# Kernel optimization log

Hardware: AMD Instinct MI355X
Metric: run time of the kernel (lower is better)

Reference implementation:

```python
import jax, jax.numpy as jnp
import numpy as np

B, C, H, W = 8, 128, 64, 64
D_STATE = 16
D_CONV = 4
EXPAND = 1.25
D_INNER = int(EXPAND * C)        # 160
DT_RANK = int(np.ceil(C / 16))   # 8


def setup_inputs() -> dict:
    key = jax.random.key(0)
    ks = jax.random.split(key, 10)
    f = lambda k, s, sc=0.02: jax.random.normal(k, s, dtype=jnp.float32) * sc
    return {
        "x": jax.random.normal(ks[0], (B, C, H, W), dtype=jnp.float32),
        "ln_g": jnp.ones((C,), jnp.float32),
        "ln_b": jnp.zeros((C,), jnp.float32),
        "in_proj_w": f(ks[1], (2 * D_INNER, C)),
        "conv_w": f(ks[2], (D_INNER, 1, D_CONV)),            # depthwise causal conv kernel
        "conv_b": jnp.zeros((D_INNER,), jnp.float32),
        "x_proj_w": f(ks[3], (DT_RANK + 2 * D_STATE, D_INNER)),
        "dt_proj_w": f(ks[4], (D_INNER, DT_RANK), 0.1),
        "dt_proj_b": f(ks[5], (D_INNER,), 0.1),
        # S4-style init: A_log = log(1..d_state) per inner channel (frozen in torch module)
        "A_log": jnp.log(jnp.tile(jnp.arange(1, D_STATE + 1, dtype=jnp.float32), (D_INNER, 1))),
        "D_param": jnp.ones((D_INNER,), jnp.float32),
        "out_proj_w": f(ks[6], (C, D_INNER)),
        "fuse_w": f(ks[7], (C, 2 * C)),                      # 1x1 conv == per-token matmul
        "scale": jnp.ones((1,), jnp.float32) * 0.1,
    }


def _layernorm(x, g, b, eps=1e-5):
    m = x.mean(-1, keepdims=True)
    v = x.var(-1, keepdims=True)
    return (x - m) * jax.lax.rsqrt(v + eps) * g + b


def _mamba(seq, in_proj_w, conv_w, conv_b, x_proj_w, dt_proj_w, dt_proj_b,
           A_log, D_param, out_proj_w):
    # seq: (B, L, C)
    Bsz, L, _ = seq.shape
    xz = jnp.einsum('blc,ec->ble', seq, in_proj_w)           # (B, L, 2*d_inner)
    xm, z = jnp.split(xz, 2, axis=-1)
    # depthwise causal conv over L, truncated to L (padding = d_conv-1 on the left)
    xc = jax.lax.conv_general_dilated(
        xm.transpose(0, 2, 1), conv_w, (1,), [(D_CONV - 1, 0)],
        feature_group_count=D_INNER, dimension_numbers=('NCH', 'OIH', 'NCH'))
    xm = jax.nn.silu((xc + conv_b[None, :, None]).transpose(0, 2, 1))  # (B, L, d_inner)
    x_dbl = jnp.einsum('bld,ed->ble', xm, x_proj_w)
    dt = x_dbl[..., :DT_RANK]
    Bm = x_dbl[..., DT_RANK:DT_RANK + D_STATE]               # (B, L, d_state)
    Cm = x_dbl[..., DT_RANK + D_STATE:]                      # (B, L, d_state)
    dt = jax.nn.softplus(jnp.einsum('blr,dr->bld', dt, dt_proj_w) + dt_proj_b)
    A = -jnp.exp(A_log)                                      # (d_inner, d_state)

    def step(h, inp):
        dt_t, B_t, C_t, x_t = inp                            # (B,d) (B,n) (B,n) (B,d)
        dA = jnp.exp(dt_t[:, :, None] * A)                   # (B, d_inner, d_state)
        h = dA * h + (dt_t * x_t)[:, :, None] * B_t[:, None, :]
        y = jnp.einsum('bdn,bn->bd', h, C_t)
        return h, y

    h0 = jnp.zeros((Bsz, D_INNER, D_STATE), dtype=seq.dtype)
    xs = (dt.transpose(1, 0, 2), Bm.transpose(1, 0, 2),
          Cm.transpose(1, 0, 2), xm.transpose(1, 0, 2))
    _, ys = jax.lax.scan(step, h0, xs)                       # ys: (L, B, d_inner)
    y = ys.transpose(1, 0, 2) + xm * D_param
    y = y * jax.nn.silu(z)
    return jnp.einsum('bld,cd->blc', y, out_proj_w)          # (B, L, C)


def reference(x, ln_g, ln_b, in_proj_w, conv_w, conv_b, x_proj_w, dt_proj_w,
              dt_proj_b, A_log, D_param, out_proj_w, fuse_w, scale):
    Bsz, Ch, Hh, Ww = x.shape
    seq = x.reshape(Bsz, Ch, Hh * Ww).transpose(0, 2, 1)     # (B, L, C) raster order
    seq_n = _layernorm(seq, ln_g, ln_b)                      # LN is per-token: commutes with flip
    args = (in_proj_w, conv_w, conv_b, x_proj_w, dt_proj_w, dt_proj_b,
            A_log, D_param, out_proj_w)
    y0 = _mamba(seq_n, *args)                                # forward raster scan
    y1 = _mamba(seq_n[:, ::-1, :], *args)[:, ::-1, :]        # reversed raster scan
    fused = jnp.einsum('blk,ck->blc', jnp.concatenate([y0, y1], axis=-1), fuse_w)
    out = seq + scale * fused                                # residual + learned scale
    return out.transpose(0, 2, 1).reshape(Bsz, Ch, Hh, Ww)
```

## Files before the change

kernel.cpp:

```cpp
#include <hip/hip_runtime.h>
#include <math.h>

#define LSEQ   4096
#define BATCH  8
#define CDIM   128
#define DIN    160
#define DSTATE 16
#define DTRANK 8
#define BLROWS (BATCH*LSEQ)
#define NCHUNK 128
#define TCH    32
#define SUBC   8
#define NSEG   16

typedef __attribute__((ext_vector_type(8))) short short8;
typedef __attribute__((ext_vector_type(8))) __bf16 bf16x8;
typedef __attribute__((ext_vector_type(4))) float float4v;

__device__ __forceinline__ float4v mfma_bf16(short8 a, short8 b, float4v c) {
  return __builtin_amdgcn_mfma_f32_16x16x32_bf16(
      __builtin_bit_cast(bf16x8, a), __builtin_bit_cast(bf16x8, b), c, 0, 0, 0);
}

__device__ __forceinline__ unsigned short f2bf(float f) {
  union { float f; unsigned u; } v; v.f = f;
  unsigned r = v.u + 0x7FFF + ((v.u >> 16) & 1);
  return (unsigned short)(r >> 16);
}
__device__ __forceinline__ float bf2f(unsigned short h) {
  union { unsigned u; float f; } v; v.u = ((unsigned)h) << 16;
  return v.f;
}

__global__ void prep_weights(const float* __restrict__ inpw, const float* __restrict__ xpw,
                             const float* __restrict__ fuse_w, const float* __restrict__ out_proj_w,
                             unsigned short* __restrict__ inpw_bf, unsigned short* __restrict__ xpw_bf,
                             unsigned short* __restrict__ W01) {
  int i = blockIdx.x * 256 + threadIdx.x;
  if (i < 320 * 128) inpw_bf[i] = f2bf(inpw[i]);
  if (i < 40 * 160)  xpw_bf[i]  = f2bf(xpw[i]);
  if (i < CDIM * DIN) {
    int d = i % DIN, c = i / DIN;
    float a0 = 0.f, a1 = 0.f;
    for (int k = 0; k < CDIM; ++k) {
      float o = out_proj_w[k * DIN + d];
      a0 += fuse_w[c * 256 + k] * o;
      a1 += fuse_w[c * 256 + 128 + k] * o;
    }
    W01[c * DIN + d] = f2bf(a0);
    W01[CDIM * DIN + c * DIN + d] = f2bf(a1);
  }
}

__global__ void ln_transpose_kernel(const float* __restrict__ x,
                                    const float* __restrict__ g,
                                    const float* __restrict__ bb,
                                    unsigned short* __restrict__ seqn) {
  __shared__ float sA[128 * 65];
  __shared__ float psum[2 * 256];
  __shared__ float mrs[2 * 64];
  int l0 = blockIdx.x * 64;
  int b  = blockIdx.y;
  int t  = threadIdx.x;
  int lsub = t & 63, crow = t >> 6;
  const float* xb = x + (size_t)b * CDIM * LSEQ;
  for (int it = 0; it < 32; ++it) {
    int c = crow + it * 4;
    sA[c * 65 + lsub] = xb[(size_t)c * LSEQ + l0 + lsub];
  }
  __syncthreads();
  float s = 0.f, ss = 0.f;
  for (int j = 0; j < 32; ++j) {
    int c = crow * 32 + j;
    float v = sA[c * 65 + lsub];
    s += v; ss += v * v;
  }
  psum[crow * 64 + lsub] = s;
  psum[256 + crow * 64 + lsub] = ss;
  __syncthreads();
  if (t < 64) {
    float su = 0.f, sq = 0.f;
    for (int p = 0; p < 4; ++p) { su += psum[p * 64 + t]; sq += psum[256 + p * 64 + t]; }
    float m = su * (1.f / 128.f);
    float var = sq * (1.f / 128.f) - m * m;
    mrs[t] = m;
    mrs[64 + t] = rsqrtf(var + 1e-5f);
  }
  __syncthreads();
  int c = t & 127, half = t >> 7;
  float gc = g[c], bc = bb[c];
  for (int it = 0; it < 32; ++it) {
    int l = it * 2 + half;
    float v = (sA[c * 65 + l] - mrs[l]) * mrs[64 + l] * gc + bc;
    seqn[((size_t)(b * LSEQ + l0 + l)) * CDIM + c] = f2bf(v);
  }
}

template<int K, bool MASKN, bool BF16OUT>
__global__ __launch_bounds__(256)
void gemm_mfma(const unsigned short* __restrict__ A0, const unsigned short* __restrict__ A1,
               const unsigned short* __restrict__ W,
               void* __restrict__ C0, void* __restrict__ C1, int N) {
  constexpr int LSTR = K + 8;
  __shared__ __align__(16) unsigned short As[64 * LSTR];
  __shared__ __align__(16) unsigned short Ws[64 * LSTR];
  const unsigned short* A = blockIdx.z ? A1 : A0;
  void* Cp = blockIdx.z ? C1 : C0;
  int m0 = blockIdx.x * 64;
  int n0 = blockIdx.y * 64;
  int t = threadIdx.x;
  constexpr int CH = 64 * K / 8;
  for (int c = t; c < CH; c += 256) {
    int row = c / (K / 8);
    int col = (c % (K / 8)) * 8;
    *(short8*)&As[row * LSTR + col] = *(const short8*)&A[(size_t)(m0 + row) * K + col];
    short8 wv = {};
    int nr = n0 + row;
    if (!MASKN || nr < N) wv = *(const short8*)&W[(size_t)nr * K + col];
    *(short8*)&Ws[row * LSTR + col] = wv;
  }
  __syncthreads();
  int lane = t & 63;
  int w = t >> 6;
  int l15 = lane & 15, quad = lane >> 4;
  float4v acc[4] = {};
#pragma unroll
  for (int kk = 0; kk < K; kk += 32) {
    short8 bfrag = *(const short8*)&Ws[(w * 16 + l15) * LSTR + kk + quad * 8];
#pragma unroll
    for (int i = 0; i < 4; ++i) {
      short8 afrag = *(const short8*)&As[(i * 16 + l15) * LSTR + kk + quad * 8];
      acc[i] = mfma_bf16(afrag, bfrag, acc[i]);
    }
  }
  int col = n0 + w * 16 + l15;
  if (MASKN && col >= N) return;
#pragma unroll
  for (int i = 0; i < 4; ++i)
#pragma unroll
    for (int r = 0; r < 4; ++r) {
      int row = m0 + i * 16 + quad * 4 + r;
      if (BF16OUT) ((unsigned short*)Cp)[(size_t)row * N + col] = f2bf(acc[i][r]);
      else         ((float*)Cp)[(size_t)row * N + col] = acc[i][r];
    }
}

__global__ void conv_silu_kernel(const unsigned short* __restrict__ xz,
                                 const float* __restrict__ cw,
                                 const float* __restrict__ cb,
                                 unsigned short* __restrict__ xm0,
                                 unsigned short* __restrict__ xm1,
                                 _Float16* __restrict__ szp) {
  int idx = blockIdx.x * 256 + threadIdx.x;
  int dir = blockIdx.y;
  if (idx >= BLROWS * 80) return;
  int dp = idx % 80;
  int bl = idx / 80;
  int l = bl % LSEQ, b = bl / LSEQ;
  int d = dp * 2;
  float w0[4], w1[4];
#pragma unroll
  for (int k = 0; k < 4; ++k) { w0[k] = cw[d * 4 + k]; w1[k] = cw[d * 4 + 4 + k]; }
  float a0 = cb[d], a1 = cb[d + 1];
  const unsigned short* base = xz + ((size_t)b * LSEQ) * 320 + d;
  if (dir == 0) {
#pragma unroll
    for (int k = 0; k < 4; ++k) {
      int lp = l - 3 + k;
      if (lp >= 0) {
        unsigned v = *(const unsigned*)&base[(size_t)lp * 320];
        a0 += w0[k] * bf2f((unsigned short)v);
        a1 += w1[k] * bf2f((unsigned short)(v >> 16));
      }
    }
  } else {
#pragma unroll
    for (int k = 0; k < 4; ++k) {
      int lp = l + 3 - k;
      if (lp < LSEQ) {
        unsigned v = *(const unsigned*)&base[(size_t)lp * 320];
        a0 += w0[k] * bf2f((unsigned short)v);
        a1 += w1[k] * bf2f((unsigned short)(v >> 16));
      }
    }
  }
  float s0 = a0 * __builtin_amdgcn_rcpf(1.f + __expf(-a0));
  float s1 = a1 * __builtin_amdgcn_rcpf(1.f + __expf(-a1));
  unsigned outv = (unsigned)f2bf(s0) | ((unsigned)f2bf(s1) << 16);
  unsigned short* xm = dir ? xm1 : xm0;
  *(unsigned*)&xm[(size_t)bl * DIN + d] = outv;
  if (dir == 0) {
    unsigned zv = *(const unsigned*)&xz[(size_t)bl * 320 + 160 + d];
    float z0 = bf2f((unsigned short)zv), z1 = bf2f((unsigned short)(zv >> 16));
    float g0 = z0 * __builtin_amdgcn_rcpf(1.f + __expf(-z0));
    float g1 = z1 * __builtin_amdgcn_rcpf(1.f + __expf(-z1));
    unsigned short h0 = __builtin_bit_cast(unsigned short, (_Float16)g0);
    unsigned short h1 = __builtin_bit_cast(unsigned short, (_Float16)g1);
    *(unsigned*)&szp[(size_t)bl * DIN + d] = (unsigned)h0 | ((unsigned)h1 << 16);
  }
}

__device__ __forceinline__ void decay_powers(float r1, float* dA) {
  float r2 = r1 * r1;
  float r4 = r2 * r2;
  float r8 = r4 * r4;
  dA[0] = r1;       dA[1] = r2;       dA[2] = r2 * r1;  dA[3] = r4;
  dA[4] = r4 * r1;  dA[5] = r4 * r2;  dA[6] = r4 * dA[2]; dA[7] = r8;
  dA[8] = r8 * r1;  dA[9] = r8 * r2;  dA[10] = r8 * dA[2]; dA[11] = r8 * r4;
  dA[12] = r8 * dA[4]; dA[13] = r8 * dA[5]; dA[14] = r8 * dA[6]; dA[15] = r8 * r8;
}

__device__ __forceinline__ const float* uniform_row(const float* base, int elem_off) {
  return base + __builtin_amdgcn_readfirstlane(elem_off);
}

__global__ void scan_passA(const float* __restrict__ xdbl0, const float* __restrict__ xdbl1,
                           const unsigned short* __restrict__ xm0v, const unsigned short* __restrict__ xm1v,
                           const float* __restrict__ dt_w, const float* __restrict__ dt_b,
                           const float* __restrict__ Dp,
                           float* __restrict__ Q, float* __restrict__ dtsum,
                           unsigned* __restrict__ yr0, unsigned* __restrict__ yr1) {
  int chunk = blockIdx.x, b = blockIdx.y, dir = blockIdx.z;
  int t = threadIdx.x;
  if (t >= DIN) return;
  const float* xdbl = dir ? xdbl1 : xdbl0;
  const unsigned short* xm = dir ? xm1v : xm0v;
  unsigned* yr = dir ? yr1 : yr0;
  int d = t;
  float dw[8];
#pragma unroll
  for (int r = 0; r < 8; ++r) dw[r] = dt_w[d * 8 + r];
  float db = dt_b[d];
  float Dd = Dp[d];
  float h[16];
#pragma unroll
  for (int n = 0; n < 16; ++n) h[n] = 0.f;
  float cum = 0.f;
  float rcum = 1.f;
  int l00 = dir ? (LSEQ - 1 - chunk * TCH) : (chunk * TCH);
  int step = dir ? -1 : 1;
  int rowbase = b * LSEQ + l00;
  unsigned* yrp = yr + (size_t)rowbase * DIN + d;
#pragma unroll 4
  for (int tt = 0; tt < TCH; ++tt) {
    int rowi = rowbase + step * tt;
    const float* xr = uniform_row(xdbl, rowi * 40);
    float xmv = bf2f(xm[(size_t)rowi * DIN + d]);
    float za = db, zb = 0.f;
#pragma unroll
    for (int r = 0; r < 8; r += 2) { za += xr[r] * dw[r]; zb += xr[r + 1] * dw[r + 1]; }
    float zz = za + zb;
    float e  = __expf(fminf(zz, 20.f));
    float dt = (zz > 20.f) ? zz : __logf(1.f + e);
    float r1 = __builtin_amdgcn_rcpf(1.f + e);
    cum += dt;
    rcum *= r1;
    float u = dt * xmv;
    float dA[16];
    decay_powers(r1, dA);
#pragma unroll
    for (int n = 0; n < 16; ++n) h[n] = dA[n] * h[n] + u * xr[8 + n];
    float y0 = xmv * Dd, y1 = 0.f, y2 = 0.f, y3 = 0.f;
#pragma unroll
    for (int n = 0; n < 4; ++n) {
      y0 += h[n]      * xr[24 + n];
      y1 += h[4 + n]  * xr[28 + n];
      y2 += h[8 + n]  * xr[32 + n];
      y3 += h[12 + n] * xr[36 + n];
    }
    float y = (y0 + y1) + (y2 + y3);
    unsigned short rch = __builtin_bit_cast(unsigned short, (_Float16)rcum);
    *yrp = (unsigned)f2bf(y) | ((unsigned)rch << 16);
    yrp += step * DIN;
  }
  size_t base = (size_t)((dir * BATCH + b) * NCHUNK + chunk);
  float4v* qp = (float4v*)&Q[base * (DIN * 16) + d * 16];
#pragma unroll
  for (int n = 0; n < 4; ++n) {
    float4v qv = { h[4 * n], h[4 * n + 1], h[4 * n + 2], h[4 * n + 3] };
    qp[n] = qv;
  }
  dtsum[base * DIN + d] = cum;
}

__global__ __launch_bounds__(256)
void scan_passB(const float* Q, const float* __restrict__ dtsum,
                float* Hinit) {
  __shared__ float sA[NSEG * 16], sQ[NSEG * 16];
  int blk = blockIdx.x;
  int d = blk % DIN;
  int rem = blk / DIN;
  int t = threadIdx.x;
  int n = t & 15, cs = t >> 4;
  float An = -(float)(n + 1);
  float a[SUBC], q[SUBC];
  float Aseg = 1.f, Qseg = 0.f;
#pragma unroll
  for (int j = 0; j < SUBC; ++j) {
    int ch = cs * SUBC + j;
    size_t base = (size_t)rem * NCHUNK + ch;
    float dsv = dtsum[base * DIN + d];
    float av = __expf(An * dsv);
    float qv = Q[base * (DIN * 16) + d * 16 + n];
    a[j] = av; q[j] = qv;
    Qseg = av * Qseg + qv;
    Aseg *= av;
  }
  sA[cs * 16 + n] = Aseg;
  sQ[cs * 16 + n] = Qseg;
  __syncthreads();
  if (t < 16) {
    float h = 0.f;
    for (int s = 0; s < NSEG; ++s) {
      float Av = sA[s * 16 + t], Qv = sQ[s * 16 + t];
      sA[s * 16 + t] = h;
      h = Av * h + Qv;
    }
  }
  __syncthreads();
  float h = sA[cs * 16 + n];
#pragma unroll
  for (int j = 0; j < SUBC; ++j) {
    int ch = cs * SUBC + j;
    size_t base = (size_t)rem * NCHUNK + ch;
    Hinit[base * (DIN * 16) + d * 16 + n] = h;
    h = a[j] * h + q[j];
  }
}

__global__ void scan_passC(const float* __restrict__ xdbl0, const float* __restrict__ xdbl1,
                           const _Float16* __restrict__ szp,
                           const float* __restrict__ Hinit,
                           const unsigned* __restrict__ yr0, const unsigned* __restrict__ yr1,
                           unsigned short* __restrict__ yg0, unsigned short* __restrict__ yg1) {
  int chunk = blockIdx.x, b = blockIdx.y, dir = blockIdx.z;
  int t = threadIdx.x;
  if (t >= DIN) return;
  const float* xdbl = dir ? xdbl1 : xdbl0;
  const unsigned* yrb = dir ? yr1 : yr0;
  unsigned short* yg = dir ? yg1 : yg0;
  int d = t;
  size_t base = (size_t)((dir * BATCH + b) * NCHUNK + chunk);
  float H0[16];
  const float4v* hp = (const float4v*)&Hinit[base * (DIN * 16) + d * 16];
#pragma unroll
  for (int n = 0; n < 4; ++n) {
    float4v hv = hp[n];
    H0[4 * n] = hv[0]; H0[4 * n + 1] = hv[1]; H0[4 * n + 2] = hv[2]; H0[4 * n + 3] = hv[3];
  }
  int l00 = dir ? (LSEQ - 1 - chunk * TCH) : (chunk * TCH);
  int step = dir ? -1 : 1;
  int rowbase = b * LSEQ + l00;
  unsigned short* ygp = yg + (size_t)rowbase * DIN + d;
#pragma unroll 2
  for (int tt = 0; tt < TCH; ++tt) {
    int rowi = rowbase + step * tt;
    const float* xr = uniform_row(xdbl, rowi * 40 + 24);
    size_t di = (size_t)rowi * DIN + d;
    unsigned v = yrb[di];
    float y = bf2f((unsigned short)v);
    float rcum = (float)__builtin_bit_cast(_Float16, (unsigned short)(v >> 16));
    float sz = (float)szp[di];
    float dA[16];
    decay_powers(rcum, dA);
    float c0 = 0.f, c1 = 0.f, c2 = 0.f, c3 = 0.f;
#pragma unroll
    for (int n = 0; n < 4; ++n) {
      c0 += xr[n]      * (dA[n]      * H0[n]);
      c1 += xr[4 + n]  * (dA[4 + n]  * H0[4 + n]);
      c2 += xr[8 + n]  * (dA[8 + n]  * H0[8 + n]);
      c3 += xr[12 + n] * (dA[12 + n] * H0[12 + n]);
    }
    float corr = (c0 + c1) + (c2 + c3);
    *ygp = f2bf((y + corr) * sz);
    ygp += step * DIN;
  }
}

__global__ __launch_bounds__(256)
void final_mfma(const unsigned short* __restrict__ yg0, const unsigned short* __restrict__ yg1,
                const unsigned short* __restrict__ W01, const float* __restrict__ x,
                const float* __restrict__ scale, float* __restrict__ out) {
  constexpr int K = DIN, LSTR = K + 8;
  __shared__ __align__(16) unsigned short As[64 * LSTR];
  __shared__ __align__(16) unsigned short Ws[64 * LSTR];
  float* sC = (float*)As;
  int m0 = blockIdx.x * 64;
  int c0 = blockIdx.y * 64;
  int b = m0 / LSEQ, l0 = m0 % LSEQ;
  int t = threadIdx.x;
  int lane = t & 63;
  int w = t >> 6;
  int l15 = lane & 15, quad = lane >> 4;
  float4v acc[4] = {};
  for (int pass = 0; pass < 2; ++pass) {
    const unsigned short* A = pass ? yg1 : yg0;
    const unsigned short* W = W01 + pass * (CDIM * K);
    if (pass) __syncthreads();
    constexpr int CH = 64 * K / 8;
    for (int c = t; c < CH; c += 256) {
      int row = c / (K / 8);
      int col = (c % (K / 8)) * 8;
      *(short8*)&As[row * LSTR + col] = *(const short8*)&A[(size_t)(m0 + row) * K + col];
      *(short8*)&Ws[row * LSTR + col] = *(const short8*)&W[(size_t)(c0 + row) * K + col];
    }
    __syncthreads();
#pragma unroll
    for (int kk = 0; kk < K; kk += 32) {
      short8 bfrag = *(const short8*)&Ws[(w * 16 + l15) * LSTR + kk + quad * 8];
#pragma unroll
      for (int i = 0; i < 4; ++i) {
        short8 afrag = *(const short8*)&As[(i * 16 + l15) * LSTR + kk + quad * 8];
        acc[i] = mfma_bf16(afrag, bfrag, acc[i]);
      }
    }
  }
  __syncthreads();
#pragma unroll
  for (int i = 0; i < 4; ++i)
#pragma unroll
    for (int r = 0; r < 4; ++r)
      sC[(i * 16 + quad * 4 + r) * 65 + w * 16 + l15] = acc[i][r];
  __syncthreads();
  float sc = scale[0];
  int ll = t & 63, cq = t >> 6;
#pragma unroll
  for (int j = 0; j < 16; ++j) {
    int cl = cq * 16 + j;
    float v = sC[ll * 65 + cl];
    size_t gi = ((size_t)(b * CDIM + c0 + cl)) * LSEQ + l0 + ll;
    out[gi] = x[gi] + sc * v;
  }
}

extern "C" void kernel_launch(void* const* d_in, const int* in_sizes, int n_in,
                              void* d_out, int out_size, void* d_ws, size_t ws_size,
                              hipStream_t stream) {
  const float* x        = (const float*)d_in[0];
  const float* ln_g     = (const float*)d_in[1];
  const float* ln_b     = (const float*)d_in[2];
  const float* in_projw = (const float*)d_in[3];
  const float* conv_w   = (const float*)d_in[4];
  const float* conv_b   = (const float*)d_in[5];
  const float* x_projw  = (const float*)d_in[6];
  const float* dt_projw = (const float*)d_in[7];
  const float* dt_projb = (const float*)d_in[8];
  const float* A_log    = (const float*)d_in[9];
  const float* D_param  = (const float*)d_in[10];
  const float* out_projw= (const float*)d_in[11];
  const float* fuse_w   = (const float*)d_in[12];
  const float* scale    = (const float*)d_in[13];
  float* out = (float*)d_out;
  (void)A_log;

  float* ws = (float*)d_ws;
  size_t off = 0;
  unsigned short* seqn_bf = (unsigned short*)(ws + off); off += (size_t)BLROWS * CDIM / 2;
  unsigned short* xz      = (unsigned short*)(ws + off); off += (size_t)BLROWS * 320 / 2;
  unsigned short* xm0 = (unsigned short*)(ws + off); off += (size_t)BLROWS * DIN / 2;
  unsigned short* xm1 = (unsigned short*)(ws + off); off += (size_t)BLROWS * DIN / 2;
  float* xdbl0 = ws + off; off += (size_t)BLROWS * 40;
  float* xdbl1 = ws + off; off += (size_t)BLROWS * 40;
  float* Q     = ws + off; off += (size_t)2 * BATCH * NCHUNK * DIN * 16;
  float* Hinit = Q;
  float* dtsum = ws + off; off += (size_t)2 * BATCH * NCHUNK * DIN;
  unsigned* yr0 = (unsigned*)(ws + off); off += (size_t)BLROWS * DIN;
  unsigned* yr1 = (unsigned*)(ws + off); off += (size_t)BLROWS * DIN;
  unsigned short* yg0 = (unsigned short*)(ws + off); off += (size_t)BLROWS * DIN / 2;
  unsigned short* yg1 = (unsigned short*)(ws + off); off += (size_t)BLROWS * DIN / 2;
  _Float16* szv = (_Float16*)(ws + off); off += (size_t)BLROWS * DIN / 2;
  unsigned short* W01bf = (unsigned short*)(ws + off); off += (size_t)2 * CDIM * DIN / 2;
  unsigned short* inpw_bf = (unsigned short*)(ws + off); off += (size_t)320 * 128 / 2;
  unsigned short* xpw_bf  = (unsigned short*)(ws + off); off += (size_t)40 * 160 / 2 + 8;

  prep_weights<<<(320 * 128 + 255) / 256, 256, 0, stream>>>(
      in_projw, x_projw, fuse_w, out_projw, inpw_bf, xpw_bf, W01bf);
  ln_transpose_kernel<<<dim3(LSEQ / 64, BATCH), 256, 0, stream>>>(x, ln_g, ln_b, seqn_bf);
  gemm_mfma<128, false, true><<<dim3(BLROWS / 64, 5, 1), 256, 0, stream>>>(
      seqn_bf, seqn_bf, inpw_bf, xz, xz, 320);
  conv_silu_kernel<<<dim3((BLROWS * 80 + 255) / 256, 2), 256, 0, stream>>>(
      xz, conv_w, conv_b, xm0, xm1, szv);
  gemm_mfma<160, true, false><<<dim3(BLROWS / 64, 1, 2), 256, 0, stream>>>(
      xm0, xm1, xpw_bf, xdbl0, xdbl1, 40);
  scan_passA<<<dim3(NCHUNK, BATCH, 2), 192, 0, stream>>>(xdbl0, xdbl1, xm0, xm1,
                                                         dt_projw, dt_projb, D_param,
                                                         Q, dtsum, yr0, yr1);
  scan_passB<<<2 * BATCH * DIN, 256, 0, stream>>>(Q, dtsum, Hinit);
  scan_passC<<<dim3(NCHUNK, BATCH, 2), 192, 0, stream>>>(xdbl0, xdbl1, szv, Hinit,
                                                         yr0, yr1, yg0, yg1);
  final_mfma<<<dim3(BLROWS / 64, CDIM / 64), 256, 0, stream>>>(yg0, yg1, W01bf, x, scale, out);
}
```

Measured before the change: 248.0 us.

## Fold dt_proj into x_proj GEMM and precompute softplus inputs for scan

Precomposes dt_proj with the dt rows of x_proj into a 192x160 weight, so the x-projection GEMM directly produces the dt pre-activation. Its epilogue applies softplus and the decay factor, then stores packed fp16 (u, r1) pairs along with separate B/C values. The scan passes stage B/C for the chunk in shared memory, prefetch per-step operands eight steps ahead, and replace the dtsum exp in pass B with powers of the cumulative decay. This removes the per-step dt projection and transcendentals from the serial scan, at the cost of a larger GEMM, extra fp16 traffic, reduced precision for u and r1, and reuse of the xz buffer for UR0.

```diff
diff --git a/kernel.cpp b/kernel.cpp
--- a/kernel.cpp
+++ b/kernel.cpp
@@ -31,14 +31,31 @@
   union { unsigned u; float f; } v; v.u = ((unsigned)h) << 16;
   return v.f;
 }
+__device__ __forceinline__ float f16tof(unsigned short h) {
+  return (float)__builtin_bit_cast(_Float16, h);
+}
+__device__ __forceinline__ unsigned short ftof16(float f) {
+  return __builtin_bit_cast(unsigned short, (_Float16)f);
+}
 
 __global__ void prep_weights(const float* __restrict__ inpw, const float* __restrict__ xpw,
+                             const float* __restrict__ dtw,
                              const float* __restrict__ fuse_w, const float* __restrict__ out_proj_w,
-                             unsigned short* __restrict__ inpw_bf, unsigned short* __restrict__ xpw_bf,
+                             unsigned short* __restrict__ inpw_bf, unsigned short* __restrict__ Wx,
                              unsigned short* __restrict__ W01) {
   int i = blockIdx.x * 256 + threadIdx.x;
   if (i < 320 * 128) inpw_bf[i] = f2bf(inpw[i]);
-  if (i < 40 * 160)  xpw_bf[i]  = f2bf(xpw[i]);
+  if (i < 192 * 160) {
+    int rw = i / 160, e = i - rw * 160;
+    float v;
+    if (rw < 160) {
+      v = 0.f;
+      for (int r = 0; r < 8; ++r) v += dtw[rw * 8 + r] * xpw[r * 160 + e];
+    } else {
+      v = xpw[(rw - 160 + 8) * 160 + e];
+    }
+    Wx[i] = f2bf(v);
+  }
   if (i < CDIM * DIN) {
     int d = i % DIN, c = i / DIN;
     float a0 = 0.f, a1 = 0.f;
@@ -145,6 +162,70 @@
     }
 }
 
+__global__ __launch_bounds__(256)
+void gemm_xproj(const unsigned short* __restrict__ A0, const unsigned short* __restrict__ A1,
+                const unsigned short* __restrict__ W, const float* __restrict__ dt_b,
+                unsigned* __restrict__ UR0, unsigned* __restrict__ UR1,
+                float* __restrict__ BCo0, float* __restrict__ BCo1) {
+  constexpr int K = DIN, LSTR = K + 8;
+  __shared__ __align__(16) unsigned short As[64 * LSTR];
+  __shared__ __align__(16) unsigned short Ws[64 * LSTR];
+  const unsigned short* A = blockIdx.z ? A1 : A0;
+  unsigned* UR = blockIdx.z ? UR1 : UR0;
+  float* BCo = blockIdx.z ? BCo1 : BCo0;
+  int m0 = blockIdx.x * 64;
+  int n0 = blockIdx.y * 64;
+  int t = threadIdx.x;
+  constexpr int CH = 64 * K / 8;
+  for (int c = t; c < CH; c += 256) {
+    int row = c / (K / 8);
+    int col = (c % (K / 8)) * 8;
+    *(short8*)&As[row * LSTR + col] = *(const short8*)&A[(size_t)(m0 + row) * K + col];
+    *(short8*)&Ws[row * LSTR + col] = *(const short8*)&W[(size_t)(n0 + row) * K + col];
+  }
+  __syncthreads();
+  int lane = t & 63;
+  int w = t >> 6;
+  int l15 = lane & 15, quad = lane >> 4;
+  float4v acc[4] = {};
+#pragma unroll
+  for (int kk = 0; kk < K; kk += 32) {
+    short8 bfrag = *(const short8*)&Ws[(w * 16 + l15) * LSTR + kk + quad * 8];
+#pragma unroll
+    for (int i = 0; i < 4; ++i) {
+      short8 afrag = *(const short8*)&As[(i * 16 + l15) * LSTR + kk + quad * 8];
+      acc[i] = mfma_bf16(afrag, bfrag, acc[i]);
+    }
+  }
+  int col = n0 + w * 16 + l15;
+  if (col < 160) {
+    float db = dt_b[col];
+#pragma unroll
+    for (int i = 0; i < 4; ++i)
+#pragma unroll
+      for (int r = 0; r < 4; ++r) {
+        int rl = i * 16 + quad * 4 + r;
+        int row = m0 + rl;
+        float zz = acc[i][r] + db;
+        float e  = __expf(fminf(zz, 20.f));
+        float dt = (zz > 20.f) ? zz : __logf(1.f + e);
+        float r1 = __builtin_amdgcn_rcpf(1.f + e);
+        float xmv = bf2f(As[rl * LSTR + col]);
+        float u = dt * xmv;
+        UR[(size_t)row * DIN + col] = (unsigned)ftof16(u) | ((unsigned)ftof16(r1) << 16);
+      }
+  } else {
+    int c2 = col - 160;
+#pragma unroll
+    for (int i = 0; i < 4; ++i)
+#pragma unroll
+      for (int r = 0; r < 4; ++r) {
+        int row = m0 + i * 16 + quad * 4 + r;
+        BCo[(size_t)row * 32 + c2] = acc[i][r];
+      }
+  }
+}
+
 __global__ void conv_silu_kernel(const unsigned short* __restrict__ xz,
                                  const float* __restrict__ cw,
                                  const float* __restrict__ cb,
@@ -194,9 +275,7 @@
     float z0 = bf2f((unsigned short)zv), z1 = bf2f((unsigned short)(zv >> 16));
     float g0 = z0 * __builtin_amdgcn_rcpf(1.f + __expf(-z0));
     float g1 = z1 * __builtin_amdgcn_rcpf(1.f + __expf(-z1));
-    unsigned short h0 = __builtin_bit_cast(unsigned short, (_Float16)g0);
-    unsigned short h1 = __builtin_bit_cast(unsigned short, (_Float16)g1);
-    *(unsigned*)&szp[(size_t)bl * DIN + d] = (unsigned)h0 | ((unsigned)h1 << 16);
+    *(unsigned*)&szp[(size_t)bl * DIN + d] = (unsigned)ftof16(g0) | ((unsigned)ftof16(g1) << 16);
   }
 }
 
@@ -210,68 +289,69 @@
   dA[12] = r8 * dA[4]; dA[13] = r8 * dA[5]; dA[14] = r8 * dA[6]; dA[15] = r8 * r8;
 }
 
-__device__ __forceinline__ const float* uniform_row(const float* base, int elem_off) {
-  return base + __builtin_amdgcn_readfirstlane(elem_off);
-}
-
-__global__ void scan_passA(const float* __restrict__ xdbl0, const float* __restrict__ xdbl1,
-                           const unsigned short* __restrict__ xm0v, const unsigned short* __restrict__ xm1v,
-                           const float* __restrict__ dt_w, const float* __restrict__ dt_b,
-                           const float* __restrict__ Dp,
-                           float* __restrict__ Q, float* __restrict__ dtsum,
-                           unsigned* __restrict__ yr0, unsigned* __restrict__ yr1) {
+__global__ __launch_bounds__(192)
+void scan_passA(const float* __restrict__ BC0, const float* __restrict__ BC1,
+                const unsigned* __restrict__ UR0, const unsigned* __restrict__ UR1,
+                const unsigned short* __restrict__ xm0v, const unsigned short* __restrict__ xm1v,
+                const float* __restrict__ Dp,
+                float* __restrict__ Q, float* __restrict__ rcf,
+                unsigned* __restrict__ yr0, unsigned* __restrict__ yr1) {
+  __shared__ __align__(16) float sBC[TCH * 32];
   int chunk = blockIdx.x, b = blockIdx.y, dir = blockIdx.z;
   int t = threadIdx.x;
-  if (t >= DIN) return;
-  const float* xdbl = dir ? xdbl1 : xdbl0;
+  const float* BC = dir ? BC1 : BC0;
+  const unsigned* UR = dir ? UR1 : UR0;
   const unsigned short* xm = dir ? xm1v : xm0v;
   unsigned* yr = dir ? yr1 : yr0;
-  int d = t;
-  float dw[8];
-#pragma unroll
-  for (int r = 0; r < 8; ++r) dw[r] = dt_w[d * 8 + r];
-  float db = dt_b[d];
-  float Dd = Dp[d];
-  float h[16];
-#pragma unroll
-  for (int n = 0; n < 16; ++n) h[n] = 0.f;
-  float cum = 0.f;
-  float rcum = 1.f;
   int l00 = dir ? (LSEQ - 1 - chunk * TCH) : (chunk * TCH);
   int step = dir ? -1 : 1;
   int rowbase = b * LSEQ + l00;
+  for (int i = t; i < TCH * 32; i += 192)
+    sBC[i] = BC[(size_t)(rowbase + step * (i >> 5)) * 32 + (i & 31)];
+  __syncthreads();
+  if (t >= DIN) return;
+  int d = t;
+  float Dd = Dp[d];
+  float h[16];
+#pragma unroll
+  for (int n = 0; n < 16; ++n) h[n] = 0.f;
+  float rcum = 1.f;
+  const unsigned* urp = UR + (size_t)rowbase * DIN + d;
+  const unsigned short* xmp = xm + (size_t)rowbase * DIN + d;
   unsigned* yrp = yr + (size_t)rowbase * DIN + d;
-#pragma unroll 4
-  for (int tt = 0; tt < TCH; ++tt) {
-    int rowi = rowbase + step * tt;
-    const float* xr = uniform_row(xdbl, rowi * 40);
-    float xmv = bf2f(xm[(size_t)rowi * DIN + d]);
-    float za = db, zb = 0.f;
-#pragma unroll
-    for (int r = 0; r < 8; r += 2) { za += xr[r] * dw[r]; zb += xr[r + 1] * dw[r + 1]; }
-    float zz = za + zb;
-    float e  = __expf(fminf(zz, 20.f));
-    float dt = (zz > 20.f) ? zz : __logf(1.f + e);
-    float r1 = __builtin_amdgcn_rcpf(1.f + e);
-    cum += dt;
-    rcum *= r1;
-    float u = dt * xmv;
-    float dA[16];
-    decay_powers(r1, dA);
-#pragma unroll
-    for (int n = 0; n < 16; ++n) h[n] = dA[n] * h[n] + u * xr[8 + n];
-    float y0 = xmv * Dd, y1 = 0.f, y2 = 0.f, y3 = 0.f;
-#pragma unroll
-    for (int n = 0; n < 4; ++n) {
-      y0 += h[n]      * xr[24 + n];
-      y1 += h[4 + n]  * xr[28 + n];
-      y2 += h[8 + n]  * xr[32 + n];
-      y3 += h[12 + n] * xr[36 + n];
-    }
-    float y = (y0 + y1) + (y2 + y3);
-    unsigned short rch = __builtin_bit_cast(unsigned short, (_Float16)rcum);
-    *yrp = (unsigned)f2bf(y) | ((unsigned)rch << 16);
-    yrp += step * DIN;
+  int sstep = step * DIN;
+  unsigned urb[8]; unsigned short xmb[8];
+#pragma unroll
+  for (int j = 0; j < 8; ++j) { urb[j] = urp[sstep * j]; xmb[j] = xmp[sstep * j]; }
+  for (int g = 0; g < TCH / 8; ++g) {
+#pragma unroll
+    for (int j = 0; j < 8; ++j) {
+      int tt = g * 8 + j;
+      unsigned urv = urb[j];
+      float xmv = bf2f(xmb[j]);
+      if (g < TCH / 8 - 1) {
+        urb[j] = urp[sstep * (tt + 8)];
+        xmb[j] = xmp[sstep * (tt + 8)];
+      }
+      float u  = f16tof((unsigned short)(urv & 0xFFFF));
+      float r1 = f16tof((unsigned short)(urv >> 16));
+      rcum *= r1;
+      float dA[16];
+      decay_powers(r1, dA);
+      const float* br = &sBC[tt * 32];
+#pragma unroll
+      for (int n = 0; n < 16; ++n) h[n] = dA[n] * h[n] + u * br[n];
+      float y0 = xmv * Dd, y1 = 0.f, y2 = 0.f, y3 = 0.f;
+#pragma unroll
+      for (int n = 0; n < 4; ++n) {
+        y0 += h[n]      * br[16 + n];
+        y1 += h[4 + n]  * br[20 + n];
+        y2 += h[8 + n]  * br[24 + n];
+        y3 += h[12 + n] * br[28 + n];
+      }
+      float y = (y0 + y1) + (y2 + y3);
+      yrp[sstep * tt] = (unsigned)f2bf(y) | ((unsigned)ftof16(rcum) << 16);
+    }
   }
   size_t base = (size_t)((dir * BATCH + b) * NCHUNK + chunk);
   float4v* qp = (float4v*)&Q[base * (DIN * 16) + d * 16];
@@ -280,11 +360,11 @@
     float4v qv = { h[4 * n], h[4 * n + 1], h[4 * n + 2], h[4 * n + 3] };
     qp[n] = qv;
   }
-  dtsum[base * DIN + d] = cum;
+  rcf[base * DIN + d] = rcum;
 }
 
 __global__ __launch_bounds__(256)
-void scan_passB(const float* Q, const float* __restrict__ dtsum,
+void scan_passB(const float* Q, const float* __restrict__ rcf,
                 float* Hinit) {
   __shared__ float sA[NSEG * 16], sQ[NSEG * 16];
   int blk = blockIdx.x;
@@ -292,15 +372,21 @@
   int rem = blk / DIN;
   int t = threadIdx.x;
   int n = t & 15, cs = t >> 4;
-  float An = -(float)(n + 1);
+  unsigned k = n + 1;
   float a[SUBC], q[SUBC];
   float Aseg = 1.f, Qseg = 0.f;
 #pragma unroll
   for (int j = 0; j < SUBC; ++j) {
     int ch = cs * SUBC + j;
     size_t base = (size_t)rem * NCHUNK + ch;
-    float dsv = dtsum[base * DIN + d];
-    float av = __expf(An * dsv);
+    float rf = rcf[base * DIN + d];
+    float r2 = rf * rf, r4 = r2 * r2, r8 = r4 * r4;
+    float av = 1.f;
+    if (k & 1) av *= rf;
+    if (k & 2) av *= r2;
+    if (k & 4) av *= r4;
+    if (k & 8) av *= r8;
+    if (k & 16) av = r8 * r8;
     float qv = Q[base * (DIN * 16) + d * 16 + n];
     a[j] = av; q[j] = qv;
     Qseg = av * Qseg + qv;
@@ -328,17 +414,25 @@
   }
 }
 
-__global__ void scan_passC(const float* __restrict__ xdbl0, const float* __restrict__ xdbl1,
-                           const _Float16* __restrict__ szp,
-                           const float* __restrict__ Hinit,
-                           const unsigned* __restrict__ yr0, const unsigned* __restrict__ yr1,
-                           unsigned short* __restrict__ yg0, unsigned short* __restrict__ yg1) {
+__global__ __launch_bounds__(192)
+void scan_passC(const float* __restrict__ BC0, const float* __restrict__ BC1,
+                const _Float16* __restrict__ szp,
+                const float* __restrict__ Hinit,
+                const unsigned* __restrict__ yr0, const unsigned* __restrict__ yr1,
+                unsigned short* __restrict__ yg0, unsigned short* __restrict__ yg1) {
+  __shared__ __align__(16) float sC[TCH * 16];
   int chunk = blockIdx.x, b = blockIdx.y, dir = blockIdx.z;
   int t = threadIdx.x;
+  const float* BC = dir ? BC1 : BC0;
+  const unsigned* yrb0 = dir ? yr1 : yr0;
+  unsigned short* yg = dir ? yg1 : yg0;
+  int l00 = dir ? (LSEQ - 1 - chunk * TCH) : (chunk * TCH);
+  int step = dir ? -1 : 1;
+  int rowbase = b * LSEQ + l00;
+  for (int i = t; i < TCH * 16; i += 192)
+    sC[i] = BC[(size_t)(rowbase + step * (i >> 4)) * 32 + 16 + (i & 15)];
+  __syncthreads();
   if (t >= DIN) return;
-  const float* xdbl = dir ? xdbl1 : xdbl0;
-  const unsigned* yrb = dir ? yr1 : yr0;
-  unsigned short* yg = dir ? yg1 : yg0;
   int d = t;
   size_t base = (size_t)((dir * BATCH + b) * NCHUNK + chunk);
   float H0[16];
@@ -348,32 +442,39 @@
     float4v hv = hp[n];
     H0[4 * n] = hv[0]; H0[4 * n + 1] = hv[1]; H0[4 * n + 2] = hv[2]; H0[4 * n + 3] = hv[3];
   }
-  int l00 = dir ? (LSEQ - 1 - chunk * TCH) : (chunk * TCH);
-  int step = dir ? -1 : 1;
-  int rowbase = b * LSEQ + l00;
+  const unsigned* yrp = yrb0 + (size_t)rowbase * DIN + d;
+  const unsigned short* szq = (const unsigned short*)szp + (size_t)rowbase * DIN + d;
   unsigned short* ygp = yg + (size_t)rowbase * DIN + d;
-#pragma unroll 2
-  for (int tt = 0; tt < TCH; ++tt) {
-    int rowi = rowbase + step * tt;
-    const float* xr = uniform_row(xdbl, rowi * 40 + 24);
-    size_t di = (size_t)rowi * DIN + d;
-    unsigned v = yrb[di];
-    float y = bf2f((unsigned short)v);
-    float rcum = (float)__builtin_bit_cast(_Float16, (unsigned short)(v >> 16));
-    float sz = (float)szp[di];
-    float dA[16];
-    decay_powers(rcum, dA);
-    float c0 = 0.f, c1 = 0.f, c2 = 0.f, c3 = 0.f;
-#pragma unroll
-    for (int n = 0; n < 4; ++n) {
-      c0 += xr[n]      * (dA[n]      * H0[n]);
-      c1 += xr[4 + n]  * (dA[4 + n]  * H0[4 + n]);
-      c2 += xr[8 + n]  * (dA[8 + n]  * H0[8 + n]);
-      c3 += xr[12 + n] * (dA[12 + n] * H0[12 + n]);
-    }
-    float corr = (c0 + c1) + (c2 + c3);
-    *ygp = f2bf((y + corr) * sz);
-    ygp += step * DIN;
+  int sstep = step * DIN;
+  unsigned yb[8]; unsigned short sb[8];
+#pragma unroll
+  for (int j = 0; j < 8; ++j) { yb[j] = yrp[sstep * j]; sb[j] = szq[sstep * j]; }
+  for (int g = 0; g < TCH / 8; ++g) {
+#pragma unroll
+    for (int j = 0; j < 8; ++j) {
+      int tt = g * 8 + j;
+      unsigned v = yb[j];
+      float sz = f16tof(sb[j]);
+      if (g < TCH / 8 - 1) {
+        yb[j] = yrp[sstep * (tt + 8)];
+        sb[j] = szq[sstep * (tt + 8)];
+      }
+      float y = bf2f((unsigned short)v);
+      float rcum = f16tof((unsigned short)(v >> 16));
+      const float* cr = &sC[tt * 16];
+      float dA[16];
+      decay_powers(rcum, dA);
+      float c0 = 0.f, c1 = 0.f, c2 = 0.f, c3 = 0.f;
+#pragma unroll
+      for (int n = 0; n < 4; ++n) {
+        c0 += cr[n]      * (dA[n]      * H0[n]);
+        c1 += cr[4 + n]  * (dA[4 + n]  * H0[4 + n]);
+        c2 += cr[8 + n]  * (dA[8 + n]  * H0[8 + n]);
+        c3 += cr[12 + n] * (dA[12 + n] * H0[12 + n]);
+      }
+      float corr = (c0 + c1) + (c2 + c3);
+      ygp[sstep * tt] = f2bf((y + corr) * sz);
+    }
   }
 }
 
@@ -457,36 +558,37 @@
   size_t off = 0;
   unsigned short* seqn_bf = (unsigned short*)(ws + off); off += (size_t)BLROWS * CDIM / 2;
   unsigned short* xz      = (unsigned short*)(ws + off); off += (size_t)BLROWS * 320 / 2;
+  unsigned* UR0 = (unsigned*)xz;
   unsigned short* xm0 = (unsigned short*)(ws + off); off += (size_t)BLROWS * DIN / 2;
   unsigned short* xm1 = (unsigned short*)(ws + off); off += (size_t)BLROWS * DIN / 2;
-  float* xdbl0 = ws + off; off += (size_t)BLROWS * 40;
-  float* xdbl1 = ws + off; off += (size_t)BLROWS * 40;
+  float* BC0 = ws + off; off += (size_t)BLROWS * 32;
+  float* BC1 = ws + off; off += (size_t)BLROWS * 32;
   float* Q     = ws + off; off += (size_t)2 * BATCH * NCHUNK * DIN * 16;
   float* Hinit = Q;
-  float* dtsum = ws + off; off += (size_t)2 * BATCH * NCHUNK * DIN;
+  float* rcf   = ws + off; off += (size_t)2 * BATCH * NCHUNK * DIN;
   unsigned* yr0 = (unsigned*)(ws + off); off += (size_t)BLROWS * DIN;
   unsigned* yr1 = (unsigned*)(ws + off); off += (size_t)BLROWS * DIN;
   unsigned short* yg0 = (unsigned short*)(ws + off); off += (size_t)BLROWS * DIN / 2;
   unsigned short* yg1 = (unsigned short*)(ws + off); off += (size_t)BLROWS * DIN / 2;
   _Float16* szv = (_Float16*)(ws + off); off += (size_t)BLROWS * DIN / 2;
+  unsigned* UR1 = (unsigned*)(ws + off); off += (size_t)BLROWS * DIN;
   unsigned short* W01bf = (unsigned short*)(ws + off); off += (size_t)2 * CDIM * DIN / 2;
   unsigned short* inpw_bf = (unsigned short*)(ws + off); off += (size_t)320 * 128 / 2;
-  unsigned short* xpw_bf  = (unsigned short*)(ws + off); off += (size_t)40 * 160 / 2 + 8;
+  unsigned short* Wx_bf   = (unsigned short*)(ws + off); off += (size_t)192 * 160 / 2 + 8;
 
   prep_weights<<<(320 * 128 + 255) / 256, 256, 0, stream>>>(
-      in_projw, x_projw, fuse_w, out_projw, inpw_bf, xpw_bf, W01bf);
+      in_projw, x_projw, dt_projw, fuse_w, out_projw, inpw_bf, Wx_bf, W01bf);
   ln_transpose_kernel<<<dim3(LSEQ / 64, BATCH), 256, 0, stream>>>(x, ln_g, ln_b, seqn_bf);
   gemm_mfma<128, false, true><<<dim3(BLROWS / 64, 5, 1), 256, 0, stream>>>(
       seqn_bf, seqn_bf, inpw_bf, xz, xz, 320);
   conv_silu_kernel<<<dim3((BLROWS * 80 + 255) / 256, 2), 256, 0, stream>>>(
       xz, conv_w, conv_b, xm0, xm1, szv);
-  gemm_mfma<160, true, false><<<dim3(BLROWS / 64, 1, 2), 256, 0, stream>>>(
-      xm0, xm1, xpw_bf, xdbl0, xdbl1, 40);
-  scan_passA<<<dim3(NCHUNK, BATCH, 2), 192, 0, stream>>>(xdbl0, xdbl1, xm0, xm1,
-                                                         dt_projw, dt_projb, D_param,
-                                                         Q, dtsum, yr0, yr1);
-  scan_passB<<<2 * BATCH * DIN, 256, 0, stream>>>(Q, dtsum, Hinit);
-  scan_passC<<<dim3(NCHUNK, BATCH, 2), 192, 0, stream>>>(xdbl0, xdbl1, szv, Hinit,
+  gemm_xproj<<<dim3(BLROWS / 64, 3, 2), 256, 0, stream>>>(
+      xm0, xm1, Wx_bf, dt_projb, UR0, UR1, BC0, BC1);
+  scan_passA<<<dim3(NCHUNK, BATCH, 2), 192, 0, stream>>>(BC0, BC1, UR0, UR1, xm0, xm1,
+                                                         D_param, Q, rcf, yr0, yr1);
+  scan_passB<<<2 * BATCH * DIN, 256, 0, stream>>>(Q, rcf, Hinit);
+  scan_passC<<<dim3(NCHUNK, BATCH, 2), 192, 0, stream>>>(BC0, BC1, szv, Hinit,
                                                          yr0, yr1, yg0, yg1);
   final_mfma<<<dim3(BLROWS / 64, CDIM / 64), 256, 0, stream>>>(yg0, yg1, W01bf, x, scale, out);
 }
```

Result: slower. 261.0 us (+5.3%).
